# Performance work log

Measured on AMD Instinct MI355X. Metric: run time of the kernel, lower is better.

The kernel has to match this reference:

```python
import jax, jax.numpy as jnp
import numpy as np

B, N, DIN, D, E, STEP = 4, 1024, 256, 256, 5, 5


def setup_inputs() -> dict:
    key = jax.random.key(0)
    ks = jax.random.split(key, 14)
    s = 0.02  # weight init scale
    inp = {
        "node_features": jax.random.normal(ks[0], (B, N, DIN), dtype=jnp.float32),
        # dense per-edge-type adjacency; scaled so messages stay in a sane range
        "adj_matrices": jax.random.uniform(ks[1], (B, E, N, N), dtype=jnp.float32) * (2.0 / N),
        "fc_in_w": jax.random.normal(ks[2], (D, DIN), dtype=jnp.float32) * s,
        "fc_in_b": jnp.zeros((D,), dtype=jnp.float32),
        "edge_w": jax.random.normal(ks[3], (E, D, D), dtype=jnp.float32) * s,
        "edge_b": jax.random.normal(ks[4], (E, D), dtype=jnp.float32) * s,
        "gru_w_ih": jax.random.normal(ks[5], (3 * D, D), dtype=jnp.float32) * s,
        "gru_w_hh": jax.random.normal(ks[6], (3 * D, D), dtype=jnp.float32) * s,
        "gru_b_ih": jnp.zeros((3 * D,), dtype=jnp.float32),
        "gru_b_hh": jnp.zeros((3 * D,), dtype=jnp.float32),
        "conv1_w": jax.random.normal(ks[7], (D, D), dtype=jnp.float32) * s,
        "conv1_b": jnp.zeros((D,), dtype=jnp.float32),
        "conv2_w": jax.random.normal(ks[8], (D, D), dtype=jnp.float32) * s,
        "conv2_b": jnp.zeros((D,), dtype=jnp.float32),
    }
    return inp


def _gru_cell(x, h, w_ih, w_hh, b_ih, b_hh):
    # torch GRUCell: gates ordered [r, z, n]
    gi = x @ w_ih.T + b_ih  # [B*N, 3D]
    gh = h @ w_hh.T + b_hh
    ir, iz, inn = jnp.split(gi, 3, axis=-1)
    hr, hz, hn = jnp.split(gh, 3, axis=-1)
    r = jax.nn.sigmoid(ir + hr)
    z = jax.nn.sigmoid(iz + hz)
    n = jnp.tanh(inn + r * hn)
    return (1.0 - z) * n + z * h


def reference(node_features, adj_matrices, fc_in_w, fc_in_b, edge_w, edge_b,
              gru_w_ih, gru_w_hh, gru_b_ih, gru_b_hh,
              conv1_w, conv1_b, conv2_w, conv2_b):
    h = node_features @ fc_in_w.T + fc_in_b  # [B, N, D]
    sum_edge_b = jnp.sum(edge_b, axis=0)  # accumulated biases over edge types
    for _ in range(STEP):
        # messages per edge type: adj_e @ h  -> [B, E, N, D]
        msgs = jnp.einsum('benm,bmd->bend', adj_matrices, h)
        # per-edge-type linear (y = x @ W_e.T) then accumulate over edge types
        acc = jnp.einsum('bend,ekd->bnk', msgs, edge_w) + sum_edge_b  # [B, N, D]
        h = _gru_cell(acc, h, gru_w_ih, gru_w_hh, gru_b_ih, gru_b_hh)
    node_states = h  # [B, N, D]
    # conv1d with kernel_size=1 over node axis == per-node linear on channels
    attn_weights = jax.nn.sigmoid(node_states @ conv1_w.T + conv1_b)  # [B, N, D]
    feats = jnp.tanh(node_states @ conv2_w.T + conv2_b)  # [B, N, D]
    graph_embedding = jnp.sum(attn_weights * feats, axis=1)  # sum over nodes -> [B, D]
    attn_map = jnp.mean(attn_weights, axis=2)  # mean over channels -> [B, N]
    return (graph_embedding, node_states, attn_map)
```

## Files before the change

### kernel.cpp

```cpp
#include <hip/hip_runtime.h>
#include <hip/hip_bf16.h>
#include <cstdint>


typedef __attribute__((ext_vector_type(8))) short bf16x8;
typedef __attribute__((ext_vector_type(4))) float f32x4;

__device__ __forceinline__ float bf2f(__hip_bfloat16 x) { return __bfloat162float(x); }
__device__ __forceinline__ __hip_bfloat16 f2bf(float x) { return __float2bfloat16(x); }
__device__ __forceinline__ short f2bs(float x) {
  __hip_bfloat16 h = __float2bfloat16(x);
  return *reinterpret_cast<short*>(&h);
}
__device__ __forceinline__ float s2f(short x) {
  __hip_bfloat16 h = *reinterpret_cast<__hip_bfloat16*>(&x);
  return __bfloat162float(h);
}

__device__ __forceinline__ bf16x8 ld8_ext(const void* base, long off, bool f32) {
  if (f32) {
    const float* p = (const float*)base + off;
    bf16x8 r;
#pragma unroll
    for (int i = 0; i < 8; ++i) r[i] = f2bs(p[i]);
    return r;
  }
  return *(const bf16x8*)((const __hip_bfloat16*)base + off);
}

__device__ __forceinline__ bf16x8 ld8_sum5(const __hip_bfloat16* part, int row, int k) {
  const long base = (long)row * 256 + (long)(row >> 10) * 1048576 + k;
  float s[8] = {0.f, 0.f, 0.f, 0.f, 0.f, 0.f, 0.f, 0.f};
#pragma unroll
  for (int e = 0; e < 5; ++e) {
    bf16x8 v = *(const bf16x8*)(part + base + e * 262144);
#pragma unroll
    for (int j = 0; j < 8; ++j) s[j] += s2f(v[j]);
  }
  bf16x8 r;
#pragma unroll
  for (int j = 0; j < 8; ++j) r[j] = f2bs(s[j]);
  return r;
}

__global__ void detect_dtype(const uint32_t* __restrict__ raw, int* __restrict__ flag) {
  __shared__ int cnt;
  if (threadIdx.x == 0) cnt = 0;
  __syncthreads();
  int c = 0;
  for (int i = threadIdx.x; i < 512; i += 256) {
    uint32_t byte = (raw[i] >> 8) & 0xFF;
    if (byte >= 0x28 && byte <= 0x40) ++c;
  }
  atomicAdd(&cnt, c);
  __syncthreads();
  if (threadIdx.x == 0) *flag = (cnt < 300) ? 1 : 0;
}

__global__ void prep_pool(const void* fcb, const void* bih, const void* bhh,
                          const void* c1b, const void* c2b, const void* edgeb,
                          const int* __restrict__ flag,
                          float* __restrict__ pool, float* __restrict__ ge,
                          float* __restrict__ am32) {
  const bool f32 = (*flag != 0);
  for (int t = threadIdx.x; t < 2560; t += 256) {
    const void* p; int i;
    if (t < 256)       { p = fcb;  i = t; }
    else if (t < 1024) { p = bih;  i = t - 256; }
    else if (t < 1792) { p = bhh;  i = t - 1024; }
    else if (t < 2048) { p = c1b;  i = t - 1792; }
    else if (t < 2304) { p = c2b;  i = t - 2048; }
    else {
      int k = t - 2304; float s = 0.f;
      for (int e = 0; e < 5; ++e)
        s += f32 ? ((const float*)edgeb)[e * 256 + k]
                 : bf2f(((const __hip_bfloat16*)edgeb)[e * 256 + k]);
      pool[t] = s; continue;
    }
    pool[t] = f32 ? ((const float*)p)[i] : bf2f(((const __hip_bfloat16*)p)[i]);
  }
  for (int t = threadIdx.x; t < 1024; t += 256) ge[t] = 0.f;
  for (int t = threadIdx.x; t < 4096; t += 256) am32[t] = 0.f;
}

__global__ void bias_gi_k(const float* __restrict__ pool,
                          const __hip_bfloat16* __restrict__ wih,
                          float* __restrict__ out) {
  const int n = blockIdx.x * 256 + threadIdx.x;
  if (n >= 768) return;
  float s = pool[256 + n];
  for (int k = 0; k < 256; ++k) s += pool[2304 + k] * bf2f(wih[n * 256 + k]);
  out[n] = s;
}

__global__ void wcvt_all(const void* fcw, const void* edw, const void* wih,
                         const void* whh, const void* c1w, const void* c2w,
                         const int* __restrict__ flag, __hip_bfloat16* __restrict__ dst) {
  const bool f32 = (*flag != 0);
  const int i = blockIdx.x * 256 + threadIdx.x;
  const void* src; int off;
  if      (i < 65536)  { src = fcw; off = i; }
  else if (i < 393216) { src = edw; off = i - 65536; }
  else if (i < 589824) { src = wih; off = i - 393216; }
  else if (i < 786432) { src = whh; off = i - 589824; }
  else if (i < 851968) { src = c1w; off = i - 786432; }
  else                 { src = c2w; off = i - 851968; }
  dst[i] = f32 ? f2bf(((const float*)src)[off])
               : ((const __hip_bfloat16*)src)[off];
}

__global__ void adj_cvt(const void* __restrict__ src, const int* __restrict__ flag,
                        __hip_bfloat16* __restrict__ dst) {
  const bool f32 = (*flag != 0);
  const long i = ((long)blockIdx.x * 256 + threadIdx.x) * 8;
  bf16x8 r;
  if (f32) {
    const float* p = (const float*)src + i;
#pragma unroll
    for (int j = 0; j < 8; ++j) r[j] = f2bs(p[j]);
  } else {
    r = *(const bf16x8*)((const __hip_bfloat16*)src + i);
  }
  *(bf16x8*)(dst + i) = r;
}

template<int OUT_MODE, bool HAS_BIAS, int A_MODE, bool DUAL>
__global__ __launch_bounds__(256)
void gemm_bt(const void* __restrict__ A, const __hip_bfloat16* __restrict__ Bt,
             const float* __restrict__ bias, void* __restrict__ Cp,
             const void* __restrict__ A2, const __hip_bfloat16* __restrict__ Bt2,
             const float* __restrict__ bias2, void* __restrict__ Cp2,
             const int* __restrict__ flag,
             int Kg, int ngrp, int lda, int ldb, int ldc,
             long aBatch, int zdivA, int zmodA,
             long bBatch, int zdivB, int zmodB,
             long cBatch, int zdivC, long aGrp, long bGrp, int zSplit)
{
  __shared__ __align__(16) __hip_bfloat16 sA[64 * 64];
  __shared__ __align__(16) __hip_bfloat16 sB[64 * 64];
  const bool af32 = (A_MODE == 1) ? (*flag != 0) : false;
  const int t = threadIdx.x;
  const int w = t >> 6;
  const int l = t & 63;
  const int m0 = blockIdx.x * 64;
  const int n0 = blockIdx.y * 64;
  int z = blockIdx.z;

  const void* Au = A; const __hip_bfloat16* Btu = Bt;
  const float* biasu = bias; void* Cpu = Cp;
  bool second = false;
  if (DUAL && z >= zSplit) {
    Au = A2; Btu = Bt2; biasu = bias2; Cpu = Cp2; z -= zSplit; second = true;
  }

  const long aOff = (long)((z / zdivA) % zmodA) * aBatch;
  const __hip_bfloat16* Bb = Btu + (long)((z / zdivB) % zmodB) * bBatch;

  const int p0 = t, p1 = t + 256;
  const int sr0 = p0 >> 3, sc0 = (p0 & 7) ^ (sr0 & 7);
  const int sr1 = p1 >> 3, sc1 = (p1 & 7) ^ (sr1 & 7);

  f32x4 acc[4];
#pragma unroll
  for (int i = 0; i < 4; ++i) acc[i] = (f32x4){0.f, 0.f, 0.f, 0.f};

  const int mrow = w * 16 + (l & 15);
  const int quad = l >> 4;

  for (int g = 0; g < ngrp; ++g) {
    const long aG = aOff + (long)g * aGrp;
    const __hip_bfloat16* Bg = Bb + (long)g * bGrp;
    for (int k0 = 0; k0 < Kg; k0 += 64) {
      bf16x8 a0, a1;
      if (A_MODE == 2 && !second) {
        a0 = ld8_sum5((const __hip_bfloat16*)Au, m0 + sr0, k0 + sc0 * 8);
        a1 = ld8_sum5((const __hip_bfloat16*)Au, m0 + sr1, k0 + sc1 * 8);
      } else if (A_MODE == 1) {
        a0 = ld8_ext(Au, aG + (long)(m0 + sr0) * lda + (k0 + sc0 * 8), af32);
        a1 = ld8_ext(Au, aG + (long)(m0 + sr1) * lda + (k0 + sc1 * 8), af32);
      } else {
        const __hip_bfloat16* Ab = (const __hip_bfloat16*)Au;
        a0 = *(const bf16x8*)(Ab + aG + (long)(m0 + sr0) * lda + (k0 + sc0 * 8));
        a1 = *(const bf16x8*)(Ab + aG + (long)(m0 + sr1) * lda + (k0 + sc1 * 8));
      }
      bf16x8 b0 = *(const bf16x8*)(Bg + (long)(n0 + sr0) * ldb + (k0 + sc0 * 8));
      bf16x8 b1 = *(const bf16x8*)(Bg + (long)(n0 + sr1) * ldb + (k0 + sc1 * 8));
      __syncthreads();
      *(bf16x8*)(sA + p0 * 8) = a0;
      *(bf16x8*)(sA + p1 * 8) = a1;
      *(bf16x8*)(sB + p0 * 8) = b0;
      *(bf16x8*)(sB + p1 * 8) = b1;
      __syncthreads();
#pragma unroll
      for (int ks = 0; ks < 2; ++ks) {
        const int cg = ks * 4 + quad;
        bf16x8 af = *(const bf16x8*)(sA + mrow * 64 + ((cg ^ (mrow & 7)) * 8));
#pragma unroll
        for (int t4 = 0; t4 < 4; ++t4) {
          const int nrow = t4 * 16 + (l & 15);
          bf16x8 bfr = *(const bf16x8*)(sB + nrow * 64 + ((cg ^ (nrow & 7)) * 8));
          acc[t4] = __builtin_amdgcn_mfma_f32_16x16x32_bf16(af, bfr, acc[t4], 0, 0, 0);
        }
      }
    }
  }

  const long cOff = (long)(z / zdivC) * cBatch;
#pragma unroll
  for (int t4 = 0; t4 < 4; ++t4) {
    const int n = n0 + t4 * 16 + (l & 15);
    float bv = 0.f;
    if (HAS_BIAS) bv = biasu[n];
#pragma unroll
    for (int r = 0; r < 4; ++r) {
      const int m = m0 + w * 16 + quad * 4 + r;
      const float v = acc[t4][r] + bv;
      if (OUT_MODE == 0)
        ((__hip_bfloat16*)Cpu)[cOff + (long)m * ldc + n] = f2bf(v);
      else
        ((float*)Cpu)[cOff + (long)m * ldc + n] = v;
    }
  }
}

__global__ void gru_gate(const __hip_bfloat16* __restrict__ gi,
                         const __hip_bfloat16* __restrict__ gh,
                         __hip_bfloat16* __restrict__ hbf,
                         void* __restrict__ ns_out, const int* __restrict__ flag)
{
  const int m = blockIdx.x;
  const int k = threadIdx.x;
  const long gb = (long)m * 768;
  const float ir = bf2f(gi[gb + k]);
  const float iz = bf2f(gi[gb + 256 + k]);
  const float inn = bf2f(gi[gb + 512 + k]);
  const float hr = bf2f(gh[gb + k]);
  const float hz = bf2f(gh[gb + 256 + k]);
  const float hn = bf2f(gh[gb + 512 + k]);
  const long hidx = (long)m * 256 + k;
  const float h = bf2f(hbf[hidx]);
  const float r = 1.f / (1.f + __expf(-(ir + hr)));
  const float zz = 1.f / (1.f + __expf(-(iz + hz)));
  const float nn = tanhf(inn + r * hn);
  const float hnew = (1.f - zz) * nn + zz * h;
  const __hip_bfloat16 hb = f2bf(hnew);
  hbf[hidx] = hb;
  if (ns_out) {
    if (*flag) ((float*)ns_out)[1024 + hidx] = hnew;
    else       ((__hip_bfloat16*)ns_out)[1024 + hidx] = hb;
  }
}

__global__ __launch_bounds__(256)
void conv_fused(const __hip_bfloat16* __restrict__ hbf,
                const __hip_bfloat16* __restrict__ c1w,
                const __hip_bfloat16* __restrict__ c2w,
                const float* __restrict__ pool,
                float* __restrict__ geg, float* __restrict__ am32)
{
  __shared__ __align__(16) __hip_bfloat16 sA[64 * 64];
  __shared__ __align__(16) __hip_bfloat16 sB1[64 * 64];
  __shared__ __align__(16) __hip_bfloat16 sB2[64 * 64];
  __shared__ float sge[64];
  __shared__ float sam[64];
  const int t = threadIdx.x, w = t >> 6, l = t & 63;
  const int m0 = blockIdx.x * 64, n0 = blockIdx.y * 64;
  if (t < 64) { sge[t] = 0.f; sam[t] = 0.f; }
  const int p0 = t, p1 = t + 256;
  const int sr0 = p0 >> 3, sc0 = (p0 & 7) ^ (sr0 & 7);
  const int sr1 = p1 >> 3, sc1 = (p1 & 7) ^ (sr1 & 7);
  f32x4 a1[4], a2[4];
#pragma unroll
  for (int i = 0; i < 4; ++i) { a1[i] = (f32x4){0,0,0,0}; a2[i] = (f32x4){0,0,0,0}; }
  const int mrow = w * 16 + (l & 15);
  const int quad = l >> 4;
  for (int k0 = 0; k0 < 256; k0 += 64) {
    bf16x8 va0 = *(const bf16x8*)(hbf + (long)(m0 + sr0) * 256 + (k0 + sc0 * 8));
    bf16x8 va1 = *(const bf16x8*)(hbf + (long)(m0 + sr1) * 256 + (k0 + sc1 * 8));
    bf16x8 vb0 = *(const bf16x8*)(c1w + (long)(n0 + sr0) * 256 + (k0 + sc0 * 8));
    bf16x8 vb1 = *(const bf16x8*)(c1w + (long)(n0 + sr1) * 256 + (k0 + sc1 * 8));
    bf16x8 vc0 = *(const bf16x8*)(c2w + (long)(n0 + sr0) * 256 + (k0 + sc0 * 8));
    bf16x8 vc1 = *(const bf16x8*)(c2w + (long)(n0 + sr1) * 256 + (k0 + sc1 * 8));
    __syncthreads();
    *(bf16x8*)(sA + p0 * 8) = va0;  *(bf16x8*)(sA + p1 * 8) = va1;
    *(bf16x8*)(sB1 + p0 * 8) = vb0; *(bf16x8*)(sB1 + p1 * 8) = vb1;
    *(bf16x8*)(sB2 + p0 * 8) = vc0; *(bf16x8*)(sB2 + p1 * 8) = vc1;
    __syncthreads();
#pragma unroll
    for (int ks = 0; ks < 2; ++ks) {
      const int cg = ks * 4 + quad;
      bf16x8 af = *(const bf16x8*)(sA + mrow * 64 + ((cg ^ (mrow & 7)) * 8));
#pragma unroll
      for (int t4 = 0; t4 < 4; ++t4) {
        const int nrow = t4 * 16 + (l & 15);
        bf16x8 b1f = *(const bf16x8*)(sB1 + nrow * 64 + ((cg ^ (nrow & 7)) * 8));
        bf16x8 b2f = *(const bf16x8*)(sB2 + nrow * 64 + ((cg ^ (nrow & 7)) * 8));
        a1[t4] = __builtin_amdgcn_mfma_f32_16x16x32_bf16(af, b1f, a1[t4], 0, 0, 0);
        a2[t4] = __builtin_amdgcn_mfma_f32_16x16x32_bf16(af, b2f, a2[t4], 0, 0, 0);
      }
    }
  }
  float asum[4] = {0.f, 0.f, 0.f, 0.f};
#pragma unroll
  for (int t4 = 0; t4 < 4; ++t4) {
    const int n = n0 + t4 * 16 + (l & 15);
    const float bb1 = pool[1792 + n], bb2 = pool[2048 + n];
    float g = 0.f;
#pragma unroll
    for (int r = 0; r < 4; ++r) {
      const float av = 1.f / (1.f + __expf(-(a1[t4][r] + bb1)));
      const float fv = tanhf(a2[t4][r] + bb2);
      g += av * fv;
      asum[r] += av;
    }
    atomicAdd(&sge[t4 * 16 + (l & 15)], g);
  }
#pragma unroll
  for (int r = 0; r < 4; ++r) atomicAdd(&sam[w * 16 + quad * 4 + r], asum[r]);
  __syncthreads();
  if (t < 64) atomicAdd(&geg[(m0 >> 10) * 256 + n0 + t], sge[t]);
  else if (t < 128) atomicAdd(&am32[m0 + (t - 64)], sam[t - 64]);
}

__global__ void finish_out(const float* __restrict__ ge, const float* __restrict__ am32,
                           void* __restrict__ dout, const int* __restrict__ flag)
{
  const int t = blockIdx.x * 256 + threadIdx.x;
  const bool f32 = (*flag != 0);
  if (t < 1024) {
    if (f32) ((float*)dout)[t] = ge[t];
    else     ((__hip_bfloat16*)dout)[t] = f2bf(ge[t]);
  } else {
    const float v = am32[t - 1024] * (1.f / 256.f);
    if (f32) ((float*)dout)[1049600 + t - 1024] = v;
    else     ((__hip_bfloat16*)dout)[1049600 + t - 1024] = f2bf(v);
  }
}

extern "C" void kernel_launch(void* const* d_in, const int* in_sizes, int n_in,
                              void* d_out, int out_size, void* d_ws, size_t ws_size,
                              hipStream_t stream) {
  (void)in_sizes; (void)n_in; (void)out_size;
  const void* node_f = d_in[0];
  const void* adj    = d_in[1];
  const void* fc_w   = d_in[2];
  const void* fc_b   = d_in[3];
  const void* edge_w = d_in[4];
  const void* edge_b = d_in[5];
  const void* w_ih   = d_in[6];
  const void* w_hh   = d_in[7];
  const void* b_ih   = d_in[8];
  const void* b_hh   = d_in[9];
  const void* c1w    = d_in[10];
  const void* c1b    = d_in[11];
  const void* c2w    = d_in[12];
  const void* c2b    = d_in[13];

  char* ws = (char*)d_ws;
  const size_t MB = (size_t)1 << 20;
  int*            flag = (int*)(ws);
  float*          bp   = (float*)(ws + 256);
  float*          ge   = (float*)(ws + 14336);
  float*          am32 = (float*)(ws + 18432);
  __hip_bfloat16* wbf  = (__hip_bfloat16*)(ws + 34816);
  __hip_bfloat16* hbf  = (__hip_bfloat16*)(ws + 1869824);
  char*           S    = ws + 3966976;
  __hip_bfloat16* heT  = (__hip_bfloat16*)(S);
  __hip_bfloat16* part = (__hip_bfloat16*)(S + 10 * MB);
  __hip_bfloat16* gi   = (__hip_bfloat16*)(S + 20 * MB);
  __hip_bfloat16* gh   = (__hip_bfloat16*)(S + 26 * MB);
  __hip_bfloat16* adjb = (__hip_bfloat16*)(ws + 40 * MB);

  const bool has_split = ws_size >= 38 * MB;
  const bool has_adjb  = ws_size >= 81 * MB;

  detect_dtype<<<1, 256, 0, stream>>>((const uint32_t*)adj, flag);
  prep_pool<<<1, 256, 0, stream>>>(fc_b, b_ih, b_hh, c1b, c2b, edge_b, flag, bp, ge, am32);
  wcvt_all<<<3584, 256, 0, stream>>>(fc_w, edge_w, w_ih, w_hh, c1w, c2w, flag, wbf);
  bias_gi_k<<<3, 256, 0, stream>>>(bp, wbf + 393216, bp + 2560);
  if (has_adjb) adj_cvt<<<10240, 256, 0, stream>>>(adj, flag, adjb);

  gemm_bt<0, true, 1, false><<<dim3(64, 4, 1), 256, 0, stream>>>(
      node_f, wbf + 0, bp + 0, hbf, nullptr, nullptr, nullptr, nullptr, flag,
      256, 1, 256, 256, 256, 0, 1, 1, 0, 1, 1, 0, 1, 0, 0, 0);

  for (int s = 0; s < 5; ++s) {
    gemm_bt<0, false, 0, false><<<dim3(4, 16, 20), 256, 0, stream>>>(
        wbf + 65536, hbf, nullptr, heT, nullptr, nullptr, nullptr, nullptr, flag,
        256, 1, 256, 256, 1024,
        65536, 1, 5, 262144, 5, 4,
        262144, 1, 0, 0, 0);
    if (has_split) {
      if (has_adjb) {
        gemm_bt<0, false, 0, false><<<dim3(16, 4, 20), 256, 0, stream>>>(
            adjb, heT, nullptr, part, nullptr, nullptr, nullptr, nullptr, flag,
            1024, 1, 1024, 1024, 256,
            1048576, 1, 20, 262144, 1, 20,
            262144, 1, 0, 0, 0);
      } else {
        gemm_bt<0, false, 1, false><<<dim3(16, 4, 20), 256, 0, stream>>>(
            adj, heT, nullptr, part, nullptr, nullptr, nullptr, nullptr, flag,
            1024, 1, 1024, 1024, 256,
            1048576, 1, 20, 262144, 1, 20,
            262144, 1, 0, 0, 0);
      }
      gemm_bt<0, true, 2, true><<<dim3(64, 12, 2), 256, 0, stream>>>(
          part, wbf + 393216, bp + 2560, gi,
          hbf,  wbf + 589824, bp + 1024, gh, flag,
          256, 1, 256, 256, 768, 0, 1, 1, 0, 1, 1, 0, 1, 0, 0, 1);
    } else {
      gemm_bt<0, true, 1, false><<<dim3(16, 4, 4), 256, 0, stream>>>(
          adj, heT, bp + 2304, part, nullptr, nullptr, nullptr, nullptr, flag,
          1024, 5, 1024, 1024, 256,
          (long)5 * 1048576, 1, 4, (long)5 * 262144, 1, 4,
          262144, 1, 1048576, 262144, 0);
      gemm_bt<0, true, 0, true><<<dim3(64, 12, 2), 256, 0, stream>>>(
          part, wbf + 393216, bp + 256, gi,
          hbf,  wbf + 589824, bp + 1024, gh, flag,
          256, 1, 256, 256, 768, 0, 1, 1, 0, 1, 1, 0, 1, 0, 0, 1);
    }
    gru_gate<<<4096, 256, 0, stream>>>(gi, gh, hbf,
                                       (s == 4) ? d_out : nullptr, flag);
  }

  conv_fused<<<dim3(64, 4), 256, 0, stream>>>(hbf, wbf + 786432, wbf + 851968,
                                              bp, ge, am32);
  finish_out<<<20, 256, 0, stream>>>(ge, am32, d_out, flag);
}
```

Measured before the change: 453.9 us.

## Use direct global-to-LDS loads in GEMMs, fold edge sum into group loop, vectorize GRU

GEMM tile loads now go straight from global memory into LDS through global_load_lds instead of through registers, in both the generic GEMM and the fused conv kernel. The five-edge-type partial-sum reduction that used to run inside the A-load is removed. The gi/gh GEMM now iterates over five K groups with bf16 accumulation replaced by fp32 MFMA accumulation across groups, using a remapped grid. The GRU gate kernel processes four channels per thread with vector loads and stores. These changes cut register staging and load instructions, at the cost of more GEMM work per tile in the gi GEMM and a changed launch grid shape.

```diff
diff --git a/kernel.cpp b/kernel.cpp
--- a/kernel.cpp
+++ b/kernel.cpp
@@ -4,6 +4,7 @@
 
 
 typedef __attribute__((ext_vector_type(8))) short bf16x8;
+typedef __attribute__((ext_vector_type(4))) short bf16x4;
 typedef __attribute__((ext_vector_type(4))) float f32x4;
 
 __device__ __forceinline__ float bf2f(__hip_bfloat16 x) { return __bfloat162float(x); }
@@ -17,6 +18,13 @@
   return __bfloat162float(h);
 }
 
+__device__ __forceinline__ void gll16(const __hip_bfloat16* g, __hip_bfloat16* lds) {
+  __builtin_amdgcn_global_load_lds(
+      (const __attribute__((address_space(1))) uint32_t*)(uintptr_t)g,
+      (__attribute__((address_space(3))) uint32_t*)(uint32_t)(uintptr_t)lds,
+      16, 0, 0);
+}
+
 __device__ __forceinline__ bf16x8 ld8_ext(const void* base, long off, bool f32) {
   if (f32) {
     const float* p = (const float*)base + off;
@@ -26,21 +34,6 @@
     return r;
   }
   return *(const bf16x8*)((const __hip_bfloat16*)base + off);
-}
-
-__device__ __forceinline__ bf16x8 ld8_sum5(const __hip_bfloat16* part, int row, int k) {
-  const long base = (long)row * 256 + (long)(row >> 10) * 1048576 + k;
-  float s[8] = {0.f, 0.f, 0.f, 0.f, 0.f, 0.f, 0.f, 0.f};
-#pragma unroll
-  for (int e = 0; e < 5; ++e) {
-    bf16x8 v = *(const bf16x8*)(part + base + e * 262144);
-#pragma unroll
-    for (int j = 0; j < 8; ++j) s[j] += s2f(v[j]);
-  }
-  bf16x8 r;
-#pragma unroll
-  for (int j = 0; j < 8; ++j) r[j] = f2bs(s[j]);
-  return r;
 }
 
 __global__ void detect_dtype(const uint32_t* __restrict__ raw, int* __restrict__ flag) {
@@ -134,7 +127,8 @@
              int Kg, int ngrp, int lda, int ldb, int ldc,
              long aBatch, int zdivA, int zmodA,
              long bBatch, int zdivB, int zmodB,
-             long cBatch, int zdivC, long aGrp, long bGrp, int zSplit)
+             long cBatch, int zdivC, long aGrp, long bGrp,
+             int zSplit, int ngrp2, long aBatch2)
 {
   __shared__ __align__(16) __hip_bfloat16 sA[64 * 64];
   __shared__ __align__(16) __hip_bfloat16 sB[64 * 64];
@@ -148,12 +142,13 @@
 
   const void* Au = A; const __hip_bfloat16* Btu = Bt;
   const float* biasu = bias; void* Cpu = Cp;
-  bool second = false;
+  int ngrpu = ngrp; long aBatchu = aBatch;
   if (DUAL && z >= zSplit) {
-    Au = A2; Btu = Bt2; biasu = bias2; Cpu = Cp2; z -= zSplit; second = true;
-  }
-
-  const long aOff = (long)((z / zdivA) % zmodA) * aBatch;
+    Au = A2; Btu = Bt2; biasu = bias2; Cpu = Cp2; z -= zSplit;
+    ngrpu = ngrp2; aBatchu = aBatch2;
+  }
+
+  const long aOff = (long)((z / zdivA) % zmodA) * aBatchu;
   const __hip_bfloat16* Bb = Btu + (long)((z / zdivB) % zmodB) * bBatch;
 
   const int p0 = t, p1 = t + 256;
@@ -167,29 +162,26 @@
   const int mrow = w * 16 + (l & 15);
   const int quad = l >> 4;
 
-  for (int g = 0; g < ngrp; ++g) {
+  for (int g = 0; g < ngrpu; ++g) {
     const long aG = aOff + (long)g * aGrp;
     const __hip_bfloat16* Bg = Bb + (long)g * bGrp;
     for (int k0 = 0; k0 < Kg; k0 += 64) {
-      bf16x8 a0, a1;
-      if (A_MODE == 2 && !second) {
-        a0 = ld8_sum5((const __hip_bfloat16*)Au, m0 + sr0, k0 + sc0 * 8);
-        a1 = ld8_sum5((const __hip_bfloat16*)Au, m0 + sr1, k0 + sc1 * 8);
-      } else if (A_MODE == 1) {
-        a0 = ld8_ext(Au, aG + (long)(m0 + sr0) * lda + (k0 + sc0 * 8), af32);
-        a1 = ld8_ext(Au, aG + (long)(m0 + sr1) * lda + (k0 + sc1 * 8), af32);
+      bf16x8 a0r, a1r;
+      if (A_MODE == 1) {
+        a0r = ld8_ext(Au, aG + (long)(m0 + sr0) * lda + (k0 + sc0 * 8), af32);
+        a1r = ld8_ext(Au, aG + (long)(m0 + sr1) * lda + (k0 + sc1 * 8), af32);
+      }
+      __syncthreads();
+      if (A_MODE == 0) {
+        const __hip_bfloat16* Ab = (const __hip_bfloat16*)Au;
+        gll16(Ab + aG + (long)(m0 + sr0) * lda + (k0 + sc0 * 8), sA + p0 * 8);
+        gll16(Ab + aG + (long)(m0 + sr1) * lda + (k0 + sc1 * 8), sA + p1 * 8);
       } else {
-        const __hip_bfloat16* Ab = (const __hip_bfloat16*)Au;
-        a0 = *(const bf16x8*)(Ab + aG + (long)(m0 + sr0) * lda + (k0 + sc0 * 8));
-        a1 = *(const bf16x8*)(Ab + aG + (long)(m0 + sr1) * lda + (k0 + sc1 * 8));
+        *(bf16x8*)(sA + p0 * 8) = a0r;
+        *(bf16x8*)(sA + p1 * 8) = a1r;
       }
-      bf16x8 b0 = *(const bf16x8*)(Bg + (long)(n0 + sr0) * ldb + (k0 + sc0 * 8));
-      bf16x8 b1 = *(const bf16x8*)(Bg + (long)(n0 + sr1) * ldb + (k0 + sc1 * 8));
-      __syncthreads();
-      *(bf16x8*)(sA + p0 * 8) = a0;
-      *(bf16x8*)(sA + p1 * 8) = a1;
-      *(bf16x8*)(sB + p0 * 8) = b0;
-      *(bf16x8*)(sB + p1 * 8) = b1;
+      gll16(Bg + (long)(n0 + sr0) * ldb + (k0 + sc0 * 8), sB + p0 * 8);
+      gll16(Bg + (long)(n0 + sr1) * ldb + (k0 + sc1 * 8), sB + p1 * 8);
       __syncthreads();
 #pragma unroll
       for (int ks = 0; ks < 2; ++ks) {
@@ -228,26 +220,32 @@
                          __hip_bfloat16* __restrict__ hbf,
                          void* __restrict__ ns_out, const int* __restrict__ flag)
 {
-  const int m = blockIdx.x;
-  const int k = threadIdx.x;
-  const long gb = (long)m * 768;
-  const float ir = bf2f(gi[gb + k]);
-  const float iz = bf2f(gi[gb + 256 + k]);
-  const float inn = bf2f(gi[gb + 512 + k]);
-  const float hr = bf2f(gh[gb + k]);
-  const float hz = bf2f(gh[gb + 256 + k]);
-  const float hn = bf2f(gh[gb + 512 + k]);
-  const long hidx = (long)m * 256 + k;
-  const float h = bf2f(hbf[hidx]);
-  const float r = 1.f / (1.f + __expf(-(ir + hr)));
-  const float zz = 1.f / (1.f + __expf(-(iz + hz)));
-  const float nn = tanhf(inn + r * hn);
-  const float hnew = (1.f - zz) * nn + zz * h;
-  const __hip_bfloat16 hb = f2bf(hnew);
-  hbf[hidx] = hb;
+  const int m = blockIdx.x * 4 + (threadIdx.x >> 6);
+  const int c = (threadIdx.x & 63) * 4;
+  const long gb = (long)m * 768 + c;
+  const bf16x4 vir = *(const bf16x4*)(gi + gb);
+  const bf16x4 viz = *(const bf16x4*)(gi + gb + 256);
+  const bf16x4 vin = *(const bf16x4*)(gi + gb + 512);
+  const bf16x4 vhr = *(const bf16x4*)(gh + gb);
+  const bf16x4 vhz = *(const bf16x4*)(gh + gb + 256);
+  const bf16x4 vhn = *(const bf16x4*)(gh + gb + 512);
+  const long hidx = (long)m * 256 + c;
+  const bf16x4 vh = *(const bf16x4*)(hbf + hidx);
+  bf16x4 vout;
+  float f4[4];
+#pragma unroll
+  for (int j = 0; j < 4; ++j) {
+    const float r = 1.f / (1.f + __expf(-(s2f(vir[j]) + s2f(vhr[j]))));
+    const float zz = 1.f / (1.f + __expf(-(s2f(viz[j]) + s2f(vhz[j]))));
+    const float nn = tanhf(s2f(vin[j]) + r * s2f(vhn[j]));
+    const float hnew = (1.f - zz) * nn + zz * s2f(vh[j]);
+    vout[j] = f2bs(hnew);
+    f4[j] = hnew;
+  }
+  *(bf16x4*)(hbf + hidx) = vout;
   if (ns_out) {
-    if (*flag) ((float*)ns_out)[1024 + hidx] = hnew;
-    else       ((__hip_bfloat16*)ns_out)[1024 + hidx] = hb;
+    if (*flag) *(float4*)((float*)ns_out + 1024 + hidx) = *(const float4*)f4;
+    else       *(bf16x4*)((__hip_bfloat16*)ns_out + 1024 + hidx) = vout;
   }
 }
 
@@ -275,16 +273,13 @@
   const int mrow = w * 16 + (l & 15);
   const int quad = l >> 4;
   for (int k0 = 0; k0 < 256; k0 += 64) {
-    bf16x8 va0 = *(const bf16x8*)(hbf + (long)(m0 + sr0) * 256 + (k0 + sc0 * 8));
-    bf16x8 va1 = *(const bf16x8*)(hbf + (long)(m0 + sr1) * 256 + (k0 + sc1 * 8));
-    bf16x8 vb0 = *(const bf16x8*)(c1w + (long)(n0 + sr0) * 256 + (k0 + sc0 * 8));
-    bf16x8 vb1 = *(const bf16x8*)(c1w + (long)(n0 + sr1) * 256 + (k0 + sc1 * 8));
-    bf16x8 vc0 = *(const bf16x8*)(c2w + (long)(n0 + sr0) * 256 + (k0 + sc0 * 8));
-    bf16x8 vc1 = *(const bf16x8*)(c2w + (long)(n0 + sr1) * 256 + (k0 + sc1 * 8));
     __syncthreads();
-    *(bf16x8*)(sA + p0 * 8) = va0;  *(bf16x8*)(sA + p1 * 8) = va1;
-    *(bf16x8*)(sB1 + p0 * 8) = vb0; *(bf16x8*)(sB1 + p1 * 8) = vb1;
-    *(bf16x8*)(sB2 + p0 * 8) = vc0; *(bf16x8*)(sB2 + p1 * 8) = vc1;
+    gll16(hbf + (long)(m0 + sr0) * 256 + (k0 + sc0 * 8), sA + p0 * 8);
+    gll16(hbf + (long)(m0 + sr1) * 256 + (k0 + sc1 * 8), sA + p1 * 8);
+    gll16(c1w + (long)(n0 + sr0) * 256 + (k0 + sc0 * 8), sB1 + p0 * 8);
+    gll16(c1w + (long)(n0 + sr1) * 256 + (k0 + sc1 * 8), sB1 + p1 * 8);
+    gll16(c2w + (long)(n0 + sr0) * 256 + (k0 + sc0 * 8), sB2 + p0 * 8);
+    gll16(c2w + (long)(n0 + sr1) * 256 + (k0 + sc1 * 8), sB2 + p1 * 8);
     __syncthreads();
 #pragma unroll
     for (int ks = 0; ks < 2; ++ks) {
@@ -382,44 +377,50 @@
 
   gemm_bt<0, true, 1, false><<<dim3(64, 4, 1), 256, 0, stream>>>(
       node_f, wbf + 0, bp + 0, hbf, nullptr, nullptr, nullptr, nullptr, flag,
-      256, 1, 256, 256, 256, 0, 1, 1, 0, 1, 1, 0, 1, 0, 0, 0);
+      256, 1, 256, 256, 256, 0, 1, 1, 0, 1, 1, 0, 1, 0, 0, 0, 1, 0);
 
   for (int s = 0; s < 5; ++s) {
     gemm_bt<0, false, 0, false><<<dim3(4, 16, 20), 256, 0, stream>>>(
         wbf + 65536, hbf, nullptr, heT, nullptr, nullptr, nullptr, nullptr, flag,
         256, 1, 256, 256, 1024,
         65536, 1, 5, 262144, 5, 4,
-        262144, 1, 0, 0, 0);
-    if (has_split) {
-      if (has_adjb) {
-        gemm_bt<0, false, 0, false><<<dim3(16, 4, 20), 256, 0, stream>>>(
-            adjb, heT, nullptr, part, nullptr, nullptr, nullptr, nullptr, flag,
-            1024, 1, 1024, 1024, 256,
-            1048576, 1, 20, 262144, 1, 20,
-            262144, 1, 0, 0, 0);
-      } else {
-        gemm_bt<0, false, 1, false><<<dim3(16, 4, 20), 256, 0, stream>>>(
-            adj, heT, nullptr, part, nullptr, nullptr, nullptr, nullptr, flag,
-            1024, 1, 1024, 1024, 256,
-            1048576, 1, 20, 262144, 1, 20,
-            262144, 1, 0, 0, 0);
-      }
-      gemm_bt<0, true, 2, true><<<dim3(64, 12, 2), 256, 0, stream>>>(
+        262144, 1, 0, 0, 0, 1, 0);
+    if (has_split && has_adjb) {
+      gemm_bt<0, false, 0, false><<<dim3(16, 4, 20), 256, 0, stream>>>(
+          adjb, heT, nullptr, part, nullptr, nullptr, nullptr, nullptr, flag,
+          1024, 1, 1024, 1024, 256,
+          1048576, 1, 20, 262144, 1, 20,
+          262144, 1, 0, 0, 0, 1, 0);
+      gemm_bt<0, true, 0, true><<<dim3(16, 12, 8), 256, 0, stream>>>(
           part, wbf + 393216, bp + 2560, gi,
           hbf,  wbf + 589824, bp + 1024, gh, flag,
-          256, 1, 256, 256, 768, 0, 1, 1, 0, 1, 1, 0, 1, 0, 0, 1);
+          256, 5, 256, 256, 768,
+          1310720, 1, 4, 0, 1, 1,
+          786432, 1, 262144, 0, 4, 1, 262144);
+    } else if (has_split) {
+      gemm_bt<0, false, 1, false><<<dim3(16, 4, 20), 256, 0, stream>>>(
+          adj, heT, nullptr, part, nullptr, nullptr, nullptr, nullptr, flag,
+          1024, 1, 1024, 1024, 256,
+          1048576, 1, 20, 262144, 1, 20,
+          262144, 1, 0, 0, 0, 1, 0);
+      gemm_bt<0, true, 0, true><<<dim3(16, 12, 8), 256, 0, stream>>>(
+          part, wbf + 393216, bp + 2560, gi,
+          hbf,  wbf + 589824, bp + 1024, gh, flag,
+          256, 5, 256, 256, 768,
+          1310720, 1, 4, 0, 1, 1,
+          786432, 1, 262144, 0, 4, 1, 262144);
     } else {
       gemm_bt<0, true, 1, false><<<dim3(16, 4, 4), 256, 0, stream>>>(
           adj, heT, bp + 2304, part, nullptr, nullptr, nullptr, nullptr, flag,
           1024, 5, 1024, 1024, 256,
           (long)5 * 1048576, 1, 4, (long)5 * 262144, 1, 4,
-          262144, 1, 1048576, 262144, 0);
+          262144, 1, 1048576, 262144, 0, 1, 0);
       gemm_bt<0, true, 0, true><<<dim3(64, 12, 2), 256, 0, stream>>>(
           part, wbf + 393216, bp + 256, gi,
           hbf,  wbf + 589824, bp + 1024, gh, flag,
-          256, 1, 256, 256, 768, 0, 1, 1, 0, 1, 1, 0, 1, 0, 0, 1);
-    }
-    gru_gate<<<4096, 256, 0, stream>>>(gi, gh, hbf,
+          256, 1, 256, 256, 768, 0, 1, 1, 0, 1, 1, 0, 1, 0, 0, 1, 1, 0);
+    }
+    gru_gate<<<1024, 256, 0, stream>>>(gi, gh, hbf,
                                        (s == 4) ? d_out : nullptr, flag);
   }
 
```

After: 477.3 us. +5.2%, slower.
